# Optimization experiments

Measured on AMD Instinct MI355X. Metric: run time of the kernel, lower is better.

## Reference

```python
import jax, jax.numpy as jnp
import numpy as np

D_EV, D_RGB, D_FUSED, D_REASON = 128, 128, 384, 384
D_INNER, D_STATE, D_CONV, DT_RANK = 2 * D_REASON, 16, 4, (D_REASON + 15) // 16
B, L = 4, 1024
LN_EPS = 1e-5


def setup_inputs() -> dict:
    key = jax.random.key(0)
    ks = jax.random.split(key, 16)
    s = lambda k, shp, scale=0.02: jax.random.normal(k, shp, jnp.float32) * scale
    inp = {
        "ev_tok": jax.random.normal(ks[0], (B, L, D_EV), jnp.float32),
        "rgb_tok": jax.random.normal(ks[1], (B, L, D_RGB), jnp.float32),
        "W_ev": s(ks[2], (D_EV, D_FUSED // 2)), "b_ev": jnp.zeros((D_FUSED // 2,), jnp.float32),
        "W_rgb": s(ks[3], (D_RGB, D_FUSED // 2)), "b_rgb": jnp.zeros((D_FUSED // 2,), jnp.float32),
        "ln_g": jnp.ones((D_FUSED,), jnp.float32), "ln_b": jnp.zeros((D_FUSED,), jnp.float32),
        "W_proj": s(ks[4], (D_FUSED, D_REASON)), "b_proj": jnp.zeros((D_REASON,), jnp.float32),
        "W_in": s(ks[5], (D_REASON, 2 * D_INNER)),
        "conv_w": s(ks[6], (D_INNER, 1, D_CONV), 0.1), "conv_b": jnp.zeros((D_INNER,), jnp.float32),
        "W_x": s(ks[7], (D_INNER, DT_RANK + 2 * D_STATE)),
        "W_dt": s(ks[8], (DT_RANK, D_INNER), 0.1), "b_dt": s(ks[9], (D_INNER,), 0.1),
        "A_log": jnp.tile(jnp.log(jnp.arange(1, D_STATE + 1, dtype=jnp.float32)), (D_INNER, 1)),
        "D_skip": jnp.ones((D_INNER,), jnp.float32),
        "W_out": s(ks[10], (D_INNER, D_REASON)),
    }
    return inp


def _selective_scan(u, delta, A, Bm, Cm, D_skip):
    # u, delta: [B,L,d]; Bm, Cm: [B,L,n]; A: [d,n]; D_skip: [d]
    deltaA = jnp.exp(delta[..., None] * A)                       # [B,L,d,n]
    deltaBu = delta[..., None] * Bm[:, :, None, :] * u[..., None]  # [B,L,d,n]

    def step(h, inp):
        dA, dBu, C_t = inp
        h = dA * h + dBu                                         # [B,d,n]
        y = jnp.einsum('bdn,bn->bd', h, C_t)
        return h, y

    h0 = jnp.zeros((u.shape[0], A.shape[0], A.shape[1]), u.dtype)
    xs = (jnp.moveaxis(deltaA, 1, 0), jnp.moveaxis(deltaBu, 1, 0), jnp.moveaxis(Cm, 1, 0))
    _, ys = jax.lax.scan(step, h0, xs)                           # [L,B,d]
    return jnp.moveaxis(ys, 0, 1) + u * D_skip


def _mamba_block(x, W_in, conv_w, conv_b, W_x, W_dt, b_dt, A_log, D_skip, W_out):
    xr = x @ W_in                                                # [B,L,2*d_inner]
    u, res = jnp.split(xr, 2, axis=-1)
    # causal depthwise conv over time
    uc = jnp.swapaxes(u, 1, 2)                                   # [B,d_inner,L]
    uc = jax.lax.conv_general_dilated(uc, conv_w, (1,), [(D_CONV - 1, 0)],
                                      dimension_numbers=('NCH', 'OIH', 'NCH'),
                                      feature_group_count=D_INNER)
    u = jax.nn.silu(jnp.swapaxes(uc, 1, 2) + conv_b)             # [B,L,d_inner]
    x_dbl = u @ W_x                                              # [B,L,dt_rank+2n]
    dt, Bm, Cm = jnp.split(x_dbl, [DT_RANK, DT_RANK + D_STATE], axis=-1)
    delta = jax.nn.softplus(dt @ W_dt + b_dt)                    # [B,L,d_inner]
    A = -jnp.exp(A_log)                                          # [d_inner,n]
    y = _selective_scan(u, delta, A, Bm, Cm, D_skip)
    y = y * jax.nn.silu(res)
    return y @ W_out


def reference(ev_tok, rgb_tok, W_ev, b_ev, W_rgb, b_rgb, ln_g, ln_b, W_proj, b_proj,
              W_in, conv_w, conv_b, W_x, W_dt, b_dt, A_log, D_skip, W_out):
    x = jnp.concatenate([ev_tok @ W_ev + b_ev, rgb_tok @ W_rgb + b_rgb], axis=-1)
    mu = jnp.mean(x, axis=-1, keepdims=True)
    var = jnp.mean(jnp.square(x - mu), axis=-1, keepdims=True)
    x = (x - mu) * jax.lax.rsqrt(var + LN_EPS) * ln_g + ln_b
    x = x @ W_proj + b_proj                                      # [B,L,d_reason]
    return _mamba_block(x, W_in, conv_w, conv_b, W_x, W_dt, b_dt, A_log, D_skip, W_out)
```

## Files before the change

kernel.cpp:

```cpp
#include <hip/hip_runtime.h>
#include <cstddef>
#include <cstdint>

#define L_SEQ 1024
#define NCHUNK 64
#define CLEN 16

typedef __bf16 bf16x8 __attribute__((ext_vector_type(8)));
typedef float f32x4 __attribute__((ext_vector_type(4)));

__device__ __forceinline__ float silu_f(float x) {
    return x / (1.f + __expf(-x));
}

__device__ __forceinline__ float exp2_fast(float x) {
    return exp2f(x);
}

__device__ __forceinline__ unsigned short f2bf(float x) {
    union { float f; unsigned int u; } v; v.f = x;
    unsigned int r = (v.u + 0x7fffu + ((v.u >> 16) & 1u)) >> 16;
    return (unsigned short)r;
}
__device__ __forceinline__ float bf2f(unsigned short h) {
    union { float f; unsigned int u; } v; v.u = ((unsigned int)h) << 16;
    return v.f;
}

template<int ACT, int WHILO>
__global__ __launch_bounds__(256)
void gemm64(const float* __restrict__ A, int lda,
            const float* __restrict__ B, int ldb,
            const float* __restrict__ bias,
            float* __restrict__ Cf,
            unsigned short* __restrict__ Chi, unsigned short* __restrict__ Clo,
            int ldc, int M, int N, int K)
{
    __shared__ float As[16][68];
    __shared__ float Bs[16][64];
    const int tid = threadIdx.x;
    const int tx = tid & 15, ty = tid >> 4;
    const int m0 = blockIdx.y * 64, n0 = blockIdx.x * 64;
    const int arow = tid >> 2, acol = (tid & 3) << 2;
    const int brow = tid >> 4, bcol = (tid & 15) << 2;
    float acc[4][4] = {};
    const float* Ap = A + (size_t)(m0 + arow) * lda + acol;
    const float* Bp = B + (size_t)brow * ldb + n0 + bcol;
    const bool bok = (n0 + bcol) < N;
    for (int k0 = 0; k0 < K; k0 += 16) {
        float4 av = make_float4(0.f, 0.f, 0.f, 0.f);
        float4 bv = make_float4(0.f, 0.f, 0.f, 0.f);
        if (k0 + acol < K) av = *(const float4*)(Ap + k0);
        if (bok && (k0 + brow) < K) bv = *(const float4*)(Bp + (size_t)k0 * ldb);
        As[acol + 0][arow] = av.x;
        As[acol + 1][arow] = av.y;
        As[acol + 2][arow] = av.z;
        As[acol + 3][arow] = av.w;
        *(float4*)&Bs[brow][bcol] = bv;
        __syncthreads();
        #pragma unroll
        for (int k = 0; k < 16; ++k) {
            float4 a4 = *(const float4*)&As[k][ty * 4];
            float4 b4 = *(const float4*)&Bs[k][tx * 4];
            float aa[4] = {a4.x, a4.y, a4.z, a4.w};
            float bb[4] = {b4.x, b4.y, b4.z, b4.w};
            #pragma unroll
            for (int i = 0; i < 4; ++i)
                #pragma unroll
                for (int j = 0; j < 4; ++j)
                    acc[i][j] = fmaf(aa[i], bb[j], acc[i][j]);
        }
        __syncthreads();
    }
    const int nn = n0 + tx * 4;
    if (nn >= N) return;
    float4 bf = make_float4(0.f, 0.f, 0.f, 0.f);
    if (bias) bf = *(const float4*)(bias + nn);
    #pragma unroll
    for (int i = 0; i < 4; ++i) {
        int m = m0 + ty * 4 + i;
        float o[4];
        o[0] = acc[i][0] + bf.x;
        o[1] = acc[i][1] + bf.y;
        o[2] = acc[i][2] + bf.z;
        o[3] = acc[i][3] + bf.w;
        if (ACT == 1) {
            #pragma unroll
            for (int j = 0; j < 4; ++j)
                o[j] = fmaxf(o[j], 0.f) + log1pf(expf(-fabsf(o[j])));
        }
        if (WHILO) {
            #pragma unroll
            for (int j = 0; j < 4; ++j) {
                unsigned short h = f2bf(o[j]);
                Chi[(size_t)m * ldc + nn + j] = h;
                Clo[(size_t)m * ldc + nn + j] = f2bf(o[j] - bf2f(h));
            }
        } else {
            *(float4*)(Cf + (size_t)m * ldc + nn) = make_float4(o[0], o[1], o[2], o[3]);
        }
    }
}

template<bool APK, bool WHILO>
__global__ __launch_bounds__(256)
void gemm_bf3(const unsigned short* __restrict__ Ahi,
              const unsigned short* __restrict__ Alo,
              const unsigned int* __restrict__ Apk, int lda,
              const unsigned short* __restrict__ Bthi,
              const unsigned short* __restrict__ Btlo,
              const float* __restrict__ bias,
              float* __restrict__ Cf,
              unsigned short* __restrict__ Chi, unsigned short* __restrict__ Clo,
              int ldc, int K)
{
    __shared__ unsigned short As[2][128][40];
    __shared__ unsigned short Bs[2][128][40];
    const int tid = threadIdx.x;
    const int lane = tid & 63;
    const int wave = tid >> 6;
    const int wm = wave >> 1, wn = wave & 1;
    const int m0 = blockIdx.y * 128, n0 = blockIdx.x * 128;
    const int srow = tid >> 1, sko = (tid & 1) * 16;

    f32x4 acc[4][4];
    #pragma unroll
    for (int i = 0; i < 4; ++i)
        #pragma unroll
        for (int j = 0; j < 4; ++j) {
            f32x4 z = {0.f, 0.f, 0.f, 0.f};
            acc[i][j] = z;
        }

    const size_t aoff = (size_t)(m0 + srow) * lda + sko;
    const size_t boff = (size_t)(n0 + srow) * K + sko;

    for (int k0 = 0; k0 < K; k0 += 32) {
        if constexpr (!APK) {
            uint4 h0 = *(const uint4*)(Ahi + aoff + k0);
            uint4 h1 = *(const uint4*)(Ahi + aoff + k0 + 8);
            uint4 l0 = *(const uint4*)(Alo + aoff + k0);
            uint4 l1 = *(const uint4*)(Alo + aoff + k0 + 8);
            *(uint4*)&As[0][srow][sko]     = h0;
            *(uint4*)&As[0][srow][sko + 8] = h1;
            *(uint4*)&As[1][srow][sko]     = l0;
            *(uint4*)&As[1][srow][sko + 8] = l1;
        } else {
            const unsigned int* ap = Apk + aoff + k0;
            uint4 p0 = *(const uint4*)(ap);
            uint4 p1 = *(const uint4*)(ap + 4);
            uint4 p2 = *(const uint4*)(ap + 8);
            uint4 p3 = *(const uint4*)(ap + 12);
            uint4 h0, h1, l0, l1;
            h0.x = (p0.x >> 16) | (p0.y & 0xffff0000u);
            h0.y = (p0.z >> 16) | (p0.w & 0xffff0000u);
            h0.z = (p1.x >> 16) | (p1.y & 0xffff0000u);
            h0.w = (p1.z >> 16) | (p1.w & 0xffff0000u);
            h1.x = (p2.x >> 16) | (p2.y & 0xffff0000u);
            h1.y = (p2.z >> 16) | (p2.w & 0xffff0000u);
            h1.z = (p3.x >> 16) | (p3.y & 0xffff0000u);
            h1.w = (p3.z >> 16) | (p3.w & 0xffff0000u);
            l0.x = (p0.x & 0xffffu) | (p0.y << 16);
            l0.y = (p0.z & 0xffffu) | (p0.w << 16);
            l0.z = (p1.x & 0xffffu) | (p1.y << 16);
            l0.w = (p1.z & 0xffffu) | (p1.w << 16);
            l1.x = (p2.x & 0xffffu) | (p2.y << 16);
            l1.y = (p2.z & 0xffffu) | (p2.w << 16);
            l1.z = (p3.x & 0xffffu) | (p3.y << 16);
            l1.w = (p3.z & 0xffffu) | (p3.w << 16);
            *(uint4*)&As[0][srow][sko]     = h0;
            *(uint4*)&As[0][srow][sko + 8] = h1;
            *(uint4*)&As[1][srow][sko]     = l0;
            *(uint4*)&As[1][srow][sko + 8] = l1;
        }
        {
            uint4 bh0 = *(const uint4*)(Bthi + boff + k0);
            uint4 bh1 = *(const uint4*)(Bthi + boff + k0 + 8);
            uint4 bl0 = *(const uint4*)(Btlo + boff + k0);
            uint4 bl1 = *(const uint4*)(Btlo + boff + k0 + 8);
            *(uint4*)&Bs[0][srow][sko]     = bh0;
            *(uint4*)&Bs[0][srow][sko + 8] = bh1;
            *(uint4*)&Bs[1][srow][sko]     = bl0;
            *(uint4*)&Bs[1][srow][sko + 8] = bl1;
        }
        __syncthreads();
        const int fr = lane & 15, kq = lane >> 4;
        bf16x8 aH[4], aL[4];
        #pragma unroll
        for (int i = 0; i < 4; ++i) {
            aH[i] = *(const bf16x8*)&As[0][wm * 64 + i * 16 + fr][kq * 8];
            aL[i] = *(const bf16x8*)&As[1][wm * 64 + i * 16 + fr][kq * 8];
        }
        #pragma unroll
        for (int j = 0; j < 4; ++j) {
            bf16x8 bH = *(const bf16x8*)&Bs[0][wn * 64 + j * 16 + fr][kq * 8];
            bf16x8 bL = *(const bf16x8*)&Bs[1][wn * 64 + j * 16 + fr][kq * 8];
            #pragma unroll
            for (int i = 0; i < 4; ++i)
                acc[i][j] = __builtin_amdgcn_mfma_f32_16x16x32_bf16(aH[i], bH, acc[i][j], 0, 0, 0);
            #pragma unroll
            for (int i = 0; i < 4; ++i)
                acc[i][j] = __builtin_amdgcn_mfma_f32_16x16x32_bf16(aL[i], bH, acc[i][j], 0, 0, 0);
            #pragma unroll
            for (int i = 0; i < 4; ++i)
                acc[i][j] = __builtin_amdgcn_mfma_f32_16x16x32_bf16(aH[i], bL, acc[i][j], 0, 0, 0);
        }
        __syncthreads();
    }
    const int col = lane & 15, rq = lane >> 4;
    #pragma unroll
    for (int j = 0; j < 4; ++j) {
        int nn = n0 + wn * 64 + j * 16 + col;
        float bv = bias ? bias[nn] : 0.f;
        #pragma unroll
        for (int i = 0; i < 4; ++i) {
            int mb = m0 + wm * 64 + i * 16 + rq * 4;
            #pragma unroll
            for (int r = 0; r < 4; ++r) {
                float o = acc[i][j][r] + bv;
                if (WHILO) {
                    unsigned short h = f2bf(o);
                    Chi[(size_t)(mb + r) * ldc + nn] = h;
                    Clo[(size_t)(mb + r) * ldc + nn] = f2bf(o - bf2f(h));
                } else {
                    Cf[(size_t)(mb + r) * ldc + nn] = o;
                }
            }
        }
    }
}

__global__ __launch_bounds__(256)
void wcvt(const float* __restrict__ W, unsigned short* __restrict__ Thi,
          unsigned short* __restrict__ Tlo, int K, int N)
{
    __shared__ float t[32][33];
    const int tid = threadIdx.x;
    const int n0 = blockIdx.x * 32, k0 = blockIdx.y * 32;
    const int r = tid >> 3, c4 = (tid & 7) * 4;
    float4 v = *(const float4*)(W + (size_t)(k0 + r) * N + n0 + c4);
    t[r][c4 + 0] = v.x; t[r][c4 + 1] = v.y; t[r][c4 + 2] = v.z; t[r][c4 + 3] = v.w;
    __syncthreads();
    unsigned short hs[4], ls[4];
    #pragma unroll
    for (int j = 0; j < 4; ++j) {
        float x = t[c4 + j][r];
        hs[j] = f2bf(x);
        ls[j] = f2bf(x - bf2f(hs[j]));
    }
    size_t o = (size_t)(n0 + r) * K + k0 + c4;
    uint2 hv, lv;
    hv.x = (unsigned)hs[0] | ((unsigned)hs[1] << 16);
    hv.y = (unsigned)hs[2] | ((unsigned)hs[3] << 16);
    lv.x = (unsigned)ls[0] | ((unsigned)ls[1] << 16);
    lv.y = (unsigned)ls[2] | ((unsigned)ls[3] << 16);
    *(uint2*)(Thi + o) = hv;
    *(uint2*)(Tlo + o) = lv;
}

__global__ __launch_bounds__(256)
void ln2(unsigned short* __restrict__ hi, unsigned short* __restrict__ lo,
         const float* __restrict__ g, const float* __restrict__ b)
{
    const int lane = threadIdx.x & 63;
    const int row = blockIdx.x * 4 + (threadIdx.x >> 6);
    unsigned short* ph = hi + (size_t)row * 384;
    unsigned short* pl = lo + (size_t)row * 384;
    float v[6];
    #pragma unroll
    for (int i = 0; i < 6; ++i) {
        int c = i * 64 + lane;
        v[i] = bf2f(ph[c]) + bf2f(pl[c]);
    }
    float s = v[0] + v[1] + v[2] + v[3] + v[4] + v[5];
    #pragma unroll
    for (int m = 32; m >= 1; m >>= 1) s += __shfl_xor(s, m);
    const float mu = s * (1.f / 384.f);
    float q = 0.f;
    #pragma unroll
    for (int i = 0; i < 6; ++i) { float dv = v[i] - mu; q = fmaf(dv, dv, q); }
    #pragma unroll
    for (int m = 32; m >= 1; m >>= 1) q += __shfl_xor(q, m);
    const float inv = 1.f / sqrtf(q * (1.f / 384.f) + 1e-5f);
    #pragma unroll
    for (int i = 0; i < 6; ++i) {
        int c = i * 64 + lane;
        float o = (v[i] - mu) * inv * g[c] + b[c];
        unsigned short h = f2bf(o);
        ph[c] = h;
        pl[c] = f2bf(o - bf2f(h));
    }
}

__global__ __launch_bounds__(256)
void conv_xdbl(const float* __restrict__ xr, const float* __restrict__ conv_w,
               const float* __restrict__ conv_b, const float* __restrict__ Wx,
               float* __restrict__ u, float* __restrict__ xdbl)
{
    __shared__ float us[8 * 772];
    const int tid = threadIdx.x;
    const int tok0 = blockIdx.x * 8;
    const int t0 = tok0 & (L_SEQ - 1);
    #pragma unroll
    for (int dd = 0; dd < 3; ++dd) {
        int d = dd * 256 + tid;
        float w0 = conv_w[d * 4 + 0], w1 = conv_w[d * 4 + 1];
        float w2 = conv_w[d * 4 + 2], w3 = conv_w[d * 4 + 3];
        float cb = conv_b[d];
        #pragma unroll
        for (int tt = 0; tt < 8; ++tt) {
            int t = t0 + tt;
            const float* base = xr + (size_t)(tok0 + tt) * 1536 + d;
            float acc = cb;
            if (t >= 3) {
                acc = fmaf(base[-3 * 1536], w0, acc);
                acc = fmaf(base[-2 * 1536], w1, acc);
                acc = fmaf(base[-1 * 1536], w2, acc);
                acc = fmaf(base[0],         w3, acc);
            } else {
                if (t >= 2) acc = fmaf(base[-2 * 1536], w1, acc);
                if (t >= 1) acc = fmaf(base[-1 * 1536], w2, acc);
                acc = fmaf(base[0], w3, acc);
            }
            float sg = silu_f(acc);
            us[tt * 772 + d] = sg;
            u[(size_t)(tok0 + tt) * 768 + d] = sg;
        }
    }
    __syncthreads();
    for (int o = tid; o < 8 * 56; o += 256) {
        int tt = o / 56, c = o % 56;
        const float* ur = &us[tt * 772];
        float acc = 0.f;
        #pragma unroll 4
        for (int d4 = 0; d4 < 768; d4 += 4) {
            float4 uv = *(const float4*)&ur[d4];
            acc = fmaf(uv.x, Wx[(d4 + 0) * 56 + c], acc);
            acc = fmaf(uv.y, Wx[(d4 + 1) * 56 + c], acc);
            acc = fmaf(uv.z, Wx[(d4 + 2) * 56 + c], acc);
            acc = fmaf(uv.w, Wx[(d4 + 3) * 56 + c], acc);
        }
        xdbl[(size_t)(tok0 + tt) * 56 + c] = acc;
    }
}

__global__ __launch_bounds__(256)
void scan_a2(const float* __restrict__ delta, const float* __restrict__ u,
             const float* __restrict__ xdbl, const float* __restrict__ A_log,
             float* __restrict__ dsum_out, float* __restrict__ Bc)
{
    __shared__ float Bsh[CLEN][16];
    const int tid = threadIdx.x;
    const int d = blockIdx.x * 256 + tid;
    const int c = blockIdx.y, b = blockIdx.z;
    const int row0 = b * L_SEQ + c * CLEN;
    {
        int t = tid >> 4, n = tid & 15;
        Bsh[t][n] = xdbl[(size_t)(row0 + t) * 56 + 24 + n];
    }
    float AL2[16];
    {
        const float* ap = A_log + d * 16;
        #pragma unroll
        for (int n = 0; n < 16; ++n)
            AL2[n] = -__expf(ap[n]) * 1.44269504f;
    }
    __syncthreads();
    float h[16];
    #pragma unroll
    for (int n = 0; n < 16; ++n) h[n] = 0.f;
    float dsum = 0.f;
    const float* dp = delta + (size_t)row0 * 768 + d;
    const float* up = u + (size_t)row0 * 768 + d;
    #pragma unroll 4
    for (int t = 0; t < CLEN; ++t) {
        float dt = dp[t * 768];
        float ut = up[t * 768];
        float du = dt * ut;
        dsum += dt;
        #pragma unroll
        for (int n = 0; n < 16; ++n) {
            float dA = exp2_fast(dt * AL2[n]);
            h[n] = fmaf(dA, h[n], du * Bsh[t][n]);
        }
    }
    dsum_out[(size_t)(b * 768 + d) * NCHUNK + c] = dsum;
    float* bcp = Bc + (((size_t)(b * 768 + d)) * NCHUNK + c) * 16;
    #pragma unroll
    for (int n = 0; n < 16; ++n) bcp[n] = h[n];
}

__global__ __launch_bounds__(256)
void scan_b2(const float* __restrict__ dsum, const float* __restrict__ A_log,
             float* __restrict__ BcHin)
{
    const size_t flat = (size_t)blockIdx.x * 256 + threadIdx.x;
    const size_t bd = flat >> 4;
    const int n = (int)(flat & 15);
    const int d = (int)(bd % 768);
    const float AL2 = -__expf(A_log[d * 16 + n]) * 1.44269504f;
    const float* dsp = dsum + bd * NCHUNK;
    const size_t base = bd * (NCHUNK * 16) + n;
    float h = 0.f;
    for (int c = 0; c < NCHUNK; ++c) {
        size_t i = base + (size_t)c * 16;
        float a = exp2_fast(AL2 * dsp[c]);
        float bb = BcHin[i];
        BcHin[i] = h;
        h = fmaf(a, h, bb);
    }
}

__global__ __launch_bounds__(256)
void scan_c2(float* __restrict__ delta, const float* __restrict__ u,
             const float* __restrict__ xdbl, const float* __restrict__ A_log,
             const float* __restrict__ Hin, const float* __restrict__ D_skip,
             const float* __restrict__ xr)
{
    __shared__ float Bsh[CLEN][16];
    __shared__ float Csh[CLEN][16];
    const int tid = threadIdx.x;
    const int d = blockIdx.x * 256 + tid;
    const int c = blockIdx.y, b = blockIdx.z;
    const int row0 = b * L_SEQ + c * CLEN;
    {
        int t = tid >> 4, n = tid & 15;
        const float* xp = xdbl + (size_t)(row0 + t) * 56;
        Bsh[t][n] = xp[24 + n];
        Csh[t][n] = xp[40 + n];
    }
    float AL2[16];
    {
        const float* ap = A_log + d * 16;
        #pragma unroll
        for (int n = 0; n < 16; ++n)
            AL2[n] = -__expf(ap[n]) * 1.44269504f;
    }
    float h[16];
    {
        const float* hp = Hin + (((size_t)(b * 768 + d)) * NCHUNK + c) * 16;
        #pragma unroll
        for (int n = 0; n < 16; ++n) h[n] = hp[n];
    }
    const float Ds = D_skip[d];
    __syncthreads();
    float* dp = delta + (size_t)row0 * 768 + d;
    const float* up = u + (size_t)row0 * 768 + d;
    const float* rp = xr + (size_t)row0 * 1536 + 768 + d;
    #pragma unroll 4
    for (int t = 0; t < CLEN; ++t) {
        float dt = dp[t * 768];
        float ut = up[t * 768];
        float du = dt * ut;
        float y = 0.f;
        #pragma unroll
        for (int n = 0; n < 16; ++n) {
            float dA = exp2_fast(dt * AL2[n]);
            h[n] = fmaf(dA, h[n], du * Bsh[t][n]);
            y = fmaf(h[n], Csh[t][n], y);
        }
        float res = rp[t * 1536];
        float gy = fmaf(ut, Ds, y) * silu_f(res);
        unsigned short h16 = f2bf(gy);
        unsigned short l16 = f2bf(gy - bf2f(h16));
        unsigned int pk = ((unsigned int)h16 << 16) | (unsigned int)l16;
        dp[t * 768] = __builtin_bit_cast(float, pk);
    }
}

extern "C" void kernel_launch(void* const* d_in, const int* in_sizes, int n_in,
                              void* d_out, int out_size, void* d_ws, size_t ws_size,
                              hipStream_t stream)
{
    const float* ev     = (const float*)d_in[0];
    const float* rgb    = (const float*)d_in[1];
    const float* W_ev   = (const float*)d_in[2];
    const float* b_ev   = (const float*)d_in[3];
    const float* W_rgb  = (const float*)d_in[4];
    const float* b_rgb  = (const float*)d_in[5];
    const float* ln_g   = (const float*)d_in[6];
    const float* ln_b   = (const float*)d_in[7];
    const float* W_proj = (const float*)d_in[8];
    const float* b_proj = (const float*)d_in[9];
    const float* W_in   = (const float*)d_in[10];
    const float* conv_w = (const float*)d_in[11];
    const float* conv_b = (const float*)d_in[12];
    const float* W_x    = (const float*)d_in[13];
    const float* W_dt   = (const float*)d_in[14];
    const float* b_dt   = (const float*)d_in[15];
    const float* A_log  = (const float*)d_in[16];
    const float* D_skip = (const float*)d_in[17];
    const float* W_out  = (const float*)d_in[18];
    float* out = (float*)d_out;

    float* ws = (float*)d_ws;
    unsigned short* xfh  = (unsigned short*)ws;
    unsigned short* xfl  = xfh + 1572864;
    float* dsum          = ws;
    unsigned short* xmmh = (unsigned short*)(ws + 1572864);
    unsigned short* xmml = xmmh + 1572864;
    float* u     = ws + 1572864;
    float* xr    = ws + 4718592;
    float* xdbl  = ws + 11010048;
    float* delta = ws + 11239424;
    float* BcHin = ws + 14385152;
    unsigned short* wtp_hi = (unsigned short*)BcHin;
    unsigned short* wtp_lo = wtp_hi + 147456;
    unsigned short* wti_hi = wtp_lo + 147456;
    unsigned short* wti_lo = wti_hi + 589824;
    unsigned short* wto_hi = (unsigned short*)(ws + 17530880);
    unsigned short* wto_lo = wto_hi + 294912;

    dim3 blk(256);

    wcvt<<<dim3(12, 12), blk, 0, stream>>>(W_proj, wtp_hi, wtp_lo, 384, 384);
    wcvt<<<dim3(48, 12), blk, 0, stream>>>(W_in,   wti_hi, wti_lo, 384, 1536);
    wcvt<<<dim3(12, 24), blk, 0, stream>>>(W_out,  wto_hi, wto_lo, 768, 384);

    gemm64<0, 1><<<dim3(3, 64), blk, 0, stream>>>(ev, 128, W_ev, 192, b_ev,
                                                  nullptr, xfh, xfl, 384, 4096, 192, 128);
    gemm64<0, 1><<<dim3(3, 64), blk, 0, stream>>>(rgb, 128, W_rgb, 192, b_rgb,
                                                  nullptr, xfh + 192, xfl + 192, 384, 4096, 192, 128);
    ln2<<<1024, blk, 0, stream>>>(xfh, xfl, ln_g, ln_b);

    gemm_bf3<false, true><<<dim3(3, 32), blk, 0, stream>>>(
        xfh, xfl, nullptr, 384, wtp_hi, wtp_lo, b_proj, nullptr, xmmh, xmml, 384, 384);
    gemm_bf3<false, false><<<dim3(12, 32), blk, 0, stream>>>(
        xmmh, xmml, nullptr, 384, wti_hi, wti_lo, nullptr, xr, nullptr, nullptr, 1536, 384);

    conv_xdbl<<<512, blk, 0, stream>>>(xr, conv_w, conv_b, W_x, u, xdbl);
    gemm64<1, 0><<<dim3(12, 64), blk, 0, stream>>>(xdbl, 56, W_dt, 768, b_dt,
                                                   delta, nullptr, nullptr, 768, 4096, 768, 24);

    scan_a2<<<dim3(3, NCHUNK, 4), blk, 0, stream>>>(delta, u, xdbl, A_log, dsum, BcHin);
    scan_b2<<<192, blk, 0, stream>>>(dsum, A_log, BcHin);
    scan_c2<<<dim3(3, NCHUNK, 4), blk, 0, stream>>>(delta, u, xdbl, A_log, BcHin, D_skip, xr);

    gemm_bf3<true, false><<<dim3(3, 32), blk, 0, stream>>>(
        nullptr, nullptr, (const unsigned int*)delta, 768, wto_hi, wto_lo, nullptr,
        out, nullptr, nullptr, 384, 768);
}
```

Baseline: 228.3 us.

## Fold W_x·W_dt into one combined weight and run x_proj plus dt on MFMA

Precomputes W_x[:, :24] @ W_dt as a 768x768 weight. Concatenates it with the B/C columns of W_x into one padded split-bf16 weight, so a single MFMA gemm produces both the B/C projections and softplus(delta) straight from the conv output. The conv kernel now stores u as a packed hi/lo bf16 pair, and the two embedding GEMMs are merged into one MFMA gemm over a concatenated block-diagonal weight. This removes the scalar x_dbl GEMM and the separate dt GEMM. In exchange it does a larger GEMM (K=768 instead of the low-rank 24), adds weight-prep kernels on every call, and can change rounding because of the reassociated product.

```diff
diff --git a/kernel.cpp b/kernel.cpp
--- a/kernel.cpp
+++ b/kernel.cpp
@@ -26,15 +26,20 @@
     union { float f; unsigned int u; } v; v.u = ((unsigned int)h) << 16;
     return v.f;
 }
-
-template<int ACT, int WHILO>
+__device__ __forceinline__ unsigned int packf(float x) {
+    unsigned short h = f2bf(x);
+    unsigned short l = f2bf(x - bf2f(h));
+    return ((unsigned int)h << 16) | (unsigned int)l;
+}
+__device__ __forceinline__ float unpackf(unsigned int pk) {
+    return bf2f((unsigned short)(pk >> 16)) + bf2f((unsigned short)(pk & 0xffffu));
+}
+
 __global__ __launch_bounds__(256)
 void gemm64(const float* __restrict__ A, int lda,
             const float* __restrict__ B, int ldb,
-            const float* __restrict__ bias,
-            float* __restrict__ Cf,
-            unsigned short* __restrict__ Chi, unsigned short* __restrict__ Clo,
-            int ldc, int M, int N, int K)
+            float* __restrict__ Cf, int ldc,
+            int M, int N, int K)
 {
     __shared__ float As[16][68];
     __shared__ float Bs[16][64];
@@ -74,35 +79,15 @@
     }
     const int nn = n0 + tx * 4;
     if (nn >= N) return;
-    float4 bf = make_float4(0.f, 0.f, 0.f, 0.f);
-    if (bias) bf = *(const float4*)(bias + nn);
     #pragma unroll
     for (int i = 0; i < 4; ++i) {
         int m = m0 + ty * 4 + i;
-        float o[4];
-        o[0] = acc[i][0] + bf.x;
-        o[1] = acc[i][1] + bf.y;
-        o[2] = acc[i][2] + bf.z;
-        o[3] = acc[i][3] + bf.w;
-        if (ACT == 1) {
-            #pragma unroll
-            for (int j = 0; j < 4; ++j)
-                o[j] = fmaxf(o[j], 0.f) + log1pf(expf(-fabsf(o[j])));
-        }
-        if (WHILO) {
-            #pragma unroll
-            for (int j = 0; j < 4; ++j) {
-                unsigned short h = f2bf(o[j]);
-                Chi[(size_t)m * ldc + nn + j] = h;
-                Clo[(size_t)m * ldc + nn + j] = f2bf(o[j] - bf2f(h));
-            }
-        } else {
-            *(float4*)(Cf + (size_t)m * ldc + nn) = make_float4(o[0], o[1], o[2], o[3]);
-        }
-    }
-}
-
-template<bool APK, bool WHILO>
+        *(float4*)(Cf + (size_t)m * ldc + nn) =
+            make_float4(acc[i][0], acc[i][1], acc[i][2], acc[i][3]);
+    }
+}
+
+template<bool APK, int EPI>
 __global__ __launch_bounds__(256)
 void gemm_bf3(const unsigned short* __restrict__ Ahi,
               const unsigned short* __restrict__ Alo,
@@ -110,7 +95,7 @@
               const unsigned short* __restrict__ Bthi,
               const unsigned short* __restrict__ Btlo,
               const float* __restrict__ bias,
-              float* __restrict__ Cf,
+              float* __restrict__ Cf, float* __restrict__ Cf2,
               unsigned short* __restrict__ Chi, unsigned short* __restrict__ Clo,
               int ldc, int K)
 {
@@ -211,19 +196,28 @@
     #pragma unroll
     for (int j = 0; j < 4; ++j) {
         int nn = n0 + wn * 64 + j * 16 + col;
-        float bv = bias ? bias[nn] : 0.f;
+        float bv = 0.f;
+        if constexpr (EPI == 0 || EPI == 1) { if (bias) bv = bias[nn]; }
+        if constexpr (EPI == 2) { if (nn >= 32 && nn < 800) bv = bias[nn - 32]; }
         #pragma unroll
         for (int i = 0; i < 4; ++i) {
             int mb = m0 + wm * 64 + i * 16 + rq * 4;
             #pragma unroll
             for (int r = 0; r < 4; ++r) {
                 float o = acc[i][j][r] + bv;
-                if (WHILO) {
+                if constexpr (EPI == 0) {
+                    Cf[(size_t)(mb + r) * ldc + nn] = o;
+                } else if constexpr (EPI == 1) {
                     unsigned short h = f2bf(o);
                     Chi[(size_t)(mb + r) * ldc + nn] = h;
                     Clo[(size_t)(mb + r) * ldc + nn] = f2bf(o - bf2f(h));
                 } else {
-                    Cf[(size_t)(mb + r) * ldc + nn] = o;
+                    if (nn < 32) {
+                        Cf2[(size_t)(mb + r) * 32 + nn] = o;
+                    } else if (nn < 800) {
+                        float sp = fmaxf(o, 0.f) + log1pf(expf(-fabsf(o)));
+                        Cf[(size_t)(mb + r) * ldc + (nn - 32)] = sp;
+                    }
                 }
             }
         }
@@ -259,6 +253,49 @@
 }
 
 __global__ __launch_bounds__(256)
+void pad_btc(const float* __restrict__ W_x,
+             unsigned short* __restrict__ Thi, unsigned short* __restrict__ Tlo)
+{
+    const int flat = blockIdx.x * 256 + threadIdx.x;
+    const int r = flat / 768, k = flat % 768;
+    const int row = (r < 32) ? r : (768 + r);
+    float val = (r < 32) ? W_x[(size_t)k * 56 + 24 + r] : 0.f;
+    unsigned short h = f2bf(val);
+    Thi[(size_t)row * 768 + k] = h;
+    Tlo[(size_t)row * 768 + k] = f2bf(val - bf2f(h));
+}
+
+__global__ __launch_bounds__(256)
+void embed_pack(const float* __restrict__ ev, const float* __restrict__ rgb,
+                unsigned int* __restrict__ apk)
+{
+    const int m = blockIdx.x, kk = threadIdx.x;
+    float val = (kk < 128) ? ev[(size_t)m * 128 + kk] : rgb[(size_t)m * 128 + kk - 128];
+    apk[(size_t)m * 256 + kk] = packf(val);
+}
+
+__global__ __launch_bounds__(256)
+void wcat_cvt(const float* __restrict__ W_ev, const float* __restrict__ W_rgb,
+              const float* __restrict__ b_ev, const float* __restrict__ b_rgb,
+              unsigned short* __restrict__ Thi, unsigned short* __restrict__ Tlo,
+              float* __restrict__ biascat)
+{
+    const int flat = blockIdx.x * 256 + threadIdx.x;
+    if (flat < 384 * 256) {
+        const int n = flat >> 8, k = flat & 255;
+        float val = 0.f;
+        if (n < 192) { if (k < 128) val = W_ev[(size_t)k * 192 + n]; }
+        else         { if (k >= 128) val = W_rgb[(size_t)(k - 128) * 192 + (n - 192)]; }
+        unsigned short h = f2bf(val);
+        Thi[flat] = h;
+        Tlo[flat] = f2bf(val - bf2f(h));
+    } else if (flat < 384 * 256 + 384) {
+        const int i = flat - 384 * 256;
+        biascat[i] = (i < 192) ? b_ev[i] : b_rgb[i - 192];
+    }
+}
+
+__global__ __launch_bounds__(256)
 void ln2(unsigned short* __restrict__ hi, unsigned short* __restrict__ lo,
          const float* __restrict__ g, const float* __restrict__ b)
 {
@@ -293,60 +330,39 @@
 }
 
 __global__ __launch_bounds__(256)
-void conv_xdbl(const float* __restrict__ xr, const float* __restrict__ conv_w,
-               const float* __restrict__ conv_b, const float* __restrict__ Wx,
-               float* __restrict__ u, float* __restrict__ xdbl)
-{
-    __shared__ float us[8 * 772];
-    const int tid = threadIdx.x;
-    const int tok0 = blockIdx.x * 8;
-    const int t0 = tok0 & (L_SEQ - 1);
-    #pragma unroll
-    for (int dd = 0; dd < 3; ++dd) {
-        int d = dd * 256 + tid;
-        float w0 = conv_w[d * 4 + 0], w1 = conv_w[d * 4 + 1];
-        float w2 = conv_w[d * 4 + 2], w3 = conv_w[d * 4 + 3];
-        float cb = conv_b[d];
-        #pragma unroll
-        for (int tt = 0; tt < 8; ++tt) {
-            int t = t0 + tt;
-            const float* base = xr + (size_t)(tok0 + tt) * 1536 + d;
-            float acc = cb;
-            if (t >= 3) {
-                acc = fmaf(base[-3 * 1536], w0, acc);
-                acc = fmaf(base[-2 * 1536], w1, acc);
-                acc = fmaf(base[-1 * 1536], w2, acc);
-                acc = fmaf(base[0],         w3, acc);
-            } else {
-                if (t >= 2) acc = fmaf(base[-2 * 1536], w1, acc);
-                if (t >= 1) acc = fmaf(base[-1 * 1536], w2, acc);
-                acc = fmaf(base[0], w3, acc);
-            }
-            float sg = silu_f(acc);
-            us[tt * 772 + d] = sg;
-            u[(size_t)(tok0 + tt) * 768 + d] = sg;
-        }
-    }
-    __syncthreads();
-    for (int o = tid; o < 8 * 56; o += 256) {
-        int tt = o / 56, c = o % 56;
-        const float* ur = &us[tt * 772];
-        float acc = 0.f;
-        #pragma unroll 4
-        for (int d4 = 0; d4 < 768; d4 += 4) {
-            float4 uv = *(const float4*)&ur[d4];
-            acc = fmaf(uv.x, Wx[(d4 + 0) * 56 + c], acc);
-            acc = fmaf(uv.y, Wx[(d4 + 1) * 56 + c], acc);
-            acc = fmaf(uv.z, Wx[(d4 + 2) * 56 + c], acc);
-            acc = fmaf(uv.w, Wx[(d4 + 3) * 56 + c], acc);
-        }
-        xdbl[(size_t)(tok0 + tt) * 56 + c] = acc;
-    }
-}
-
-__global__ __launch_bounds__(256)
-void scan_a2(const float* __restrict__ delta, const float* __restrict__ u,
-             const float* __restrict__ xdbl, const float* __restrict__ A_log,
+void conv_pack(const float* __restrict__ xr, const float* __restrict__ conv_w,
+               const float* __restrict__ conv_b, unsigned int* __restrict__ upk)
+{
+    const int d = blockIdx.x * 256 + threadIdx.x;
+    const int t0 = blockIdx.z * L_SEQ + blockIdx.y * 16;
+    const float w0 = conv_w[d * 4 + 0], w1 = conv_w[d * 4 + 1];
+    const float w2 = conv_w[d * 4 + 2], w3 = conv_w[d * 4 + 3];
+    const float cb = conv_b[d];
+    const float* xp = xr + (size_t)t0 * 1536 + d;
+    float x1, x2, x3;
+    if (blockIdx.y == 0) { x1 = x2 = x3 = 0.f; }
+    else {
+        x1 = xp[-1 * 1536];
+        x2 = xp[-2 * 1536];
+        x3 = xp[-3 * 1536];
+    }
+    unsigned int* op = upk + (size_t)t0 * 768 + d;
+    #pragma unroll 4
+    for (int i = 0; i < 16; ++i) {
+        float cur = xp[i * 1536];
+        float a = cb;
+        a = fmaf(x3, w0, a);
+        a = fmaf(x2, w1, a);
+        a = fmaf(x1, w2, a);
+        a = fmaf(cur, w3, a);
+        op[i * 768] = packf(silu_f(a));
+        x3 = x2; x2 = x1; x1 = cur;
+    }
+}
+
+__global__ __launch_bounds__(256)
+void scan_a2(const float* __restrict__ delta, const unsigned int* __restrict__ upk,
+             const float* __restrict__ bc, const float* __restrict__ A_log,
              float* __restrict__ dsum_out, float* __restrict__ Bc)
 {
     __shared__ float Bsh[CLEN][16];
@@ -356,7 +372,7 @@
     const int row0 = b * L_SEQ + c * CLEN;
     {
         int t = tid >> 4, n = tid & 15;
-        Bsh[t][n] = xdbl[(size_t)(row0 + t) * 56 + 24 + n];
+        Bsh[t][n] = bc[(size_t)(row0 + t) * 32 + n];
     }
     float AL2[16];
     {
@@ -371,11 +387,11 @@
     for (int n = 0; n < 16; ++n) h[n] = 0.f;
     float dsum = 0.f;
     const float* dp = delta + (size_t)row0 * 768 + d;
-    const float* up = u + (size_t)row0 * 768 + d;
+    const unsigned int* up = upk + (size_t)row0 * 768 + d;
     #pragma unroll 4
     for (int t = 0; t < CLEN; ++t) {
         float dt = dp[t * 768];
-        float ut = up[t * 768];
+        float ut = unpackf(up[t * 768]);
         float du = dt * ut;
         dsum += dt;
         #pragma unroll
@@ -412,8 +428,8 @@
 }
 
 __global__ __launch_bounds__(256)
-void scan_c2(float* __restrict__ delta, const float* __restrict__ u,
-             const float* __restrict__ xdbl, const float* __restrict__ A_log,
+void scan_c2(float* __restrict__ delta, const unsigned int* __restrict__ upk,
+             const float* __restrict__ bc, const float* __restrict__ A_log,
              const float* __restrict__ Hin, const float* __restrict__ D_skip,
              const float* __restrict__ xr)
 {
@@ -425,9 +441,9 @@
     const int row0 = b * L_SEQ + c * CLEN;
     {
         int t = tid >> 4, n = tid & 15;
-        const float* xp = xdbl + (size_t)(row0 + t) * 56;
-        Bsh[t][n] = xp[24 + n];
-        Csh[t][n] = xp[40 + n];
+        const float* xp = bc + (size_t)(row0 + t) * 32;
+        Bsh[t][n] = xp[n];
+        Csh[t][n] = xp[16 + n];
     }
     float AL2[16];
     {
@@ -445,12 +461,12 @@
     const float Ds = D_skip[d];
     __syncthreads();
     float* dp = delta + (size_t)row0 * 768 + d;
-    const float* up = u + (size_t)row0 * 768 + d;
+    const unsigned int* up = upk + (size_t)row0 * 768 + d;
     const float* rp = xr + (size_t)row0 * 1536 + 768 + d;
     #pragma unroll 4
     for (int t = 0; t < CLEN; ++t) {
         float dt = dp[t * 768];
-        float ut = up[t * 768];
+        float ut = unpackf(up[t * 768]);
         float du = dt * ut;
         float y = 0.f;
         #pragma unroll
@@ -461,10 +477,7 @@
         }
         float res = rp[t * 1536];
         float gy = fmaf(ut, Ds, y) * silu_f(res);
-        unsigned short h16 = f2bf(gy);
-        unsigned short l16 = f2bf(gy - bf2f(h16));
-        unsigned int pk = ((unsigned int)h16 << 16) | (unsigned int)l16;
-        dp[t * 768] = __builtin_bit_cast(float, pk);
+        dp[t * 768] = __builtin_bit_cast(float, packf(gy));
     }
 }
 
@@ -497,17 +510,24 @@
     unsigned short* xfh  = (unsigned short*)ws;
     unsigned short* xfl  = xfh + 1572864;
     float* dsum          = ws;
+    float* bc            = ws + 196608;
     unsigned short* xmmh = (unsigned short*)(ws + 1572864);
     unsigned short* xmml = xmmh + 1572864;
-    float* u     = ws + 1572864;
-    float* xr    = ws + 4718592;
-    float* xdbl  = ws + 11010048;
-    float* delta = ws + 11239424;
-    float* BcHin = ws + 14385152;
+    unsigned int* upk    = (unsigned int*)(ws + 1572864);
+    float* xr            = ws + 4718592;
+    unsigned int* apk    = (unsigned int*)xr;
+    float* delta         = ws + 11239424;
+    float* BcHin         = ws + 14385152;
     unsigned short* wtp_hi = (unsigned short*)BcHin;
     unsigned short* wtp_lo = wtp_hi + 147456;
     unsigned short* wti_hi = wtp_lo + 147456;
     unsigned short* wti_lo = wti_hi + 589824;
+    float* Wcf             = BcHin + 737280;
+    unsigned short* btc_hi = (unsigned short*)(BcHin + 1327104);
+    unsigned short* btc_lo = btc_hi + 688128;
+    unsigned short* wct_hi = (unsigned short*)(BcHin + 2015232);
+    unsigned short* wct_lo = wct_hi + 98304;
+    float* biascat         = BcHin + 2113536;
     unsigned short* wto_hi = (unsigned short*)(ws + 17530880);
     unsigned short* wto_lo = wto_hi + 294912;
 
@@ -516,27 +536,30 @@
     wcvt<<<dim3(12, 12), blk, 0, stream>>>(W_proj, wtp_hi, wtp_lo, 384, 384);
     wcvt<<<dim3(48, 12), blk, 0, stream>>>(W_in,   wti_hi, wti_lo, 384, 1536);
     wcvt<<<dim3(12, 24), blk, 0, stream>>>(W_out,  wto_hi, wto_lo, 768, 384);
-
-    gemm64<0, 1><<<dim3(3, 64), blk, 0, stream>>>(ev, 128, W_ev, 192, b_ev,
-                                                  nullptr, xfh, xfl, 384, 4096, 192, 128);
-    gemm64<0, 1><<<dim3(3, 64), blk, 0, stream>>>(rgb, 128, W_rgb, 192, b_rgb,
-                                                  nullptr, xfh + 192, xfl + 192, 384, 4096, 192, 128);
+    gemm64<<<dim3(12, 12), blk, 0, stream>>>(W_x, 56, W_dt, 768, Wcf, 768, 768, 768, 24);
+    pad_btc<<<384, blk, 0, stream>>>(W_x, btc_hi, btc_lo);
+    wcvt<<<dim3(24, 24), blk, 0, stream>>>(Wcf, btc_hi + 32 * 768, btc_lo + 32 * 768, 768, 768);
+    embed_pack<<<4096, blk, 0, stream>>>(ev, rgb, apk);
+    wcat_cvt<<<386, blk, 0, stream>>>(W_ev, W_rgb, b_ev, b_rgb, wct_hi, wct_lo, biascat);
+
+    gemm_bf3<true, 1><<<dim3(3, 32), blk, 0, stream>>>(
+        nullptr, nullptr, apk, 256, wct_hi, wct_lo, biascat,
+        nullptr, nullptr, xfh, xfl, 384, 256);
     ln2<<<1024, blk, 0, stream>>>(xfh, xfl, ln_g, ln_b);
-
-    gemm_bf3<false, true><<<dim3(3, 32), blk, 0, stream>>>(
-        xfh, xfl, nullptr, 384, wtp_hi, wtp_lo, b_proj, nullptr, xmmh, xmml, 384, 384);
-    gemm_bf3<false, false><<<dim3(12, 32), blk, 0, stream>>>(
-        xmmh, xmml, nullptr, 384, wti_hi, wti_lo, nullptr, xr, nullptr, nullptr, 1536, 384);
-
-    conv_xdbl<<<512, blk, 0, stream>>>(xr, conv_w, conv_b, W_x, u, xdbl);
-    gemm64<1, 0><<<dim3(12, 64), blk, 0, stream>>>(xdbl, 56, W_dt, 768, b_dt,
-                                                   delta, nullptr, nullptr, 768, 4096, 768, 24);
-
-    scan_a2<<<dim3(3, NCHUNK, 4), blk, 0, stream>>>(delta, u, xdbl, A_log, dsum, BcHin);
+    gemm_bf3<false, 1><<<dim3(3, 32), blk, 0, stream>>>(
+        xfh, xfl, nullptr, 384, wtp_hi, wtp_lo, b_proj,
+        nullptr, nullptr, xmmh, xmml, 384, 384);
+    gemm_bf3<false, 0><<<dim3(12, 32), blk, 0, stream>>>(
+        xmmh, xmml, nullptr, 384, wti_hi, wti_lo, nullptr,
+        xr, nullptr, nullptr, nullptr, 1536, 384);
+    conv_pack<<<dim3(3, 64, 4), blk, 0, stream>>>(xr, conv_w, conv_b, upk);
+    gemm_bf3<true, 2><<<dim3(7, 32), blk, 0, stream>>>(
+        nullptr, nullptr, upk, 768, btc_hi, btc_lo, b_dt,
+        delta, bc, nullptr, nullptr, 768, 768);
+    scan_a2<<<dim3(3, NCHUNK, 4), blk, 0, stream>>>(delta, upk, bc, A_log, dsum, BcHin);
     scan_b2<<<192, blk, 0, stream>>>(dsum, A_log, BcHin);
-    scan_c2<<<dim3(3, NCHUNK, 4), blk, 0, stream>>>(delta, u, xdbl, A_log, BcHin, D_skip, xr);
-
-    gemm_bf3<true, false><<<dim3(3, 32), blk, 0, stream>>>(
+    scan_c2<<<dim3(3, NCHUNK, 4), blk, 0, stream>>>(delta, upk, bc, A_log, BcHin, D_skip, xr);
+    gemm_bf3<true, 0><<<dim3(3, 32), blk, 0, stream>>>(
         nullptr, nullptr, (const unsigned int*)delta, 768, wto_hi, wto_lo, nullptr,
-        out, nullptr, nullptr, 384, 768);
-}
+        out, nullptr, nullptr, nullptr, 384, 768);
+}
```

After: 262.6 us. 1.15x slower.
